# Kernel optimization log

Hardware: AMD Instinct MI355X
Metric: run time of the kernel (lower is better)

The kernel has to match this reference:

```python
import jax, jax.numpy as jnp
import numpy as np

B, S, D, H, L, DFF, WIN = 2, 2048, 768, 12, 2, 3072, 512
EPS = 1e-5
DH = D // H


def setup_inputs() -> dict:
    key = jax.random.key(0)
    ks = jax.random.split(key, 8)
    rn = lambda k, shape: jax.random.normal(k, shape, jnp.float32) * 0.02
    inp = {
        "src": jax.random.normal(ks[0], (B, S, D), jnp.float32),
        "qw": rn(ks[1], (L, D, D)), "qb": jnp.zeros((L, D), jnp.float32),
        "kw": rn(ks[2], (L, D, D)), "kb": jnp.zeros((L, D), jnp.float32),
        "vw": rn(ks[3], (L, D, D)), "vb": jnp.zeros((L, D), jnp.float32),
        "ow": rn(ks[4], (L, D, D)), "ob": jnp.zeros((L, D), jnp.float32),
        "w1": rn(ks[5], (L, DFF, D)), "b1": jnp.zeros((L, DFF), jnp.float32),
        "w2": rn(ks[6], (L, D, DFF)), "b2": jnp.zeros((L, D), jnp.float32),
        "g1": jnp.ones((L, D), jnp.float32), "be1": jnp.zeros((L, D), jnp.float32),
        "g2": jnp.ones((L, D), jnp.float32), "be2": jnp.zeros((L, D), jnp.float32),
    }
    return inp


def _ln(x, g, b):
    m = jnp.mean(x, axis=-1, keepdims=True)
    v = jnp.mean(jnp.square(x - m), axis=-1, keepdims=True)
    return (x - m) * jax.lax.rsqrt(v + EPS) * g + b


def _encoder(src, qw, qb, kw, kb, vw, vb, ow, ob, w1, b1, w2, b2, g1, be1, g2, be2):
    scale = DH ** -0.5
    idx = jnp.arange(S)
    # non-causal sliding window: |i - j| <= window_size // 2
    band = jnp.abs(idx[:, None] - idx[None, :]) <= (WIN // 2)
    neg = -jnp.finfo(jnp.float32).max
    x = src
    for l in range(L):
        # projections -> (B, H, S, DH)
        q = (x @ qw[l].T + qb[l]).reshape(B, S, H, DH).transpose(0, 2, 1, 3)
        k = (x @ kw[l].T + kb[l]).reshape(B, S, H, DH).transpose(0, 2, 1, 3)
        v = (x @ vw[l].T + vb[l]).reshape(B, S, H, DH).transpose(0, 2, 1, 3)
        # full dense scores then band mask (faithful to the original module)
        sim = jnp.einsum('bhid,bhjd->bhij', q * scale, k)
        sim = jnp.where(band, sim, neg)
        attn = jax.nn.softmax(sim, axis=-1)
        o = jnp.einsum('bhij,bhjd->bhid', attn, v)
        o = o.transpose(0, 2, 1, 3).reshape(B, S, D) @ ow[l].T + ob[l]
        # post-norm transformer block (norm_first=False)
        x = _ln(x + o, g1[l], be1[l])
        ff = jax.nn.relu(x @ w1[l].T + b1[l]) @ w2[l].T + b2[l]
        x = _ln(x + ff, g2[l], be2[l])
    return x


def reference(src, qw, qb, kw, kb, vw, vb, ow, ob, w1, b1, w2, b2, g1, be1, g2, be2):
    return _encoder(src, qw, qb, kw, kb, vw, vb, ow, ob, w1, b1, w2, b2, g1, be1, g2, be2)
```

## Files before the change

### kernel.cpp

```cpp
#include <hip/hip_runtime.h>
#include <math.h>

#define BATCH 2
#define SEQ   2048
#define DM    768
#define NHD   12
#define NL    2
#define DFF   3072
#define DH    64
#define HW    256
#define MR    (BATCH*SEQ)
#define EPSF  1e-5f
#define SCALE 0.125f
#define QKVS  2304

typedef __attribute__((ext_vector_type(8))) __bf16 bf16x8;
typedef __attribute__((ext_vector_type(4))) float  f32x4;

__device__ __forceinline__ ushort f2bu(float f) {
    union { __bf16 h; ushort u; } c;
    c.h = (__bf16)f;
    return c.u;
}
__device__ __forceinline__ float bu2f(ushort u) {
    union { uint u; float f; } c;
    c.u = ((uint)u) << 16;
    return c.f;
}

__device__ __forceinline__ void gload16(const ushort* g, ushort* l) {
    __builtin_amdgcn_global_load_lds(
        (const __attribute__((address_space(1))) void*)g,
        (__attribute__((address_space(3))) void*)l, 16, 0, 0);
}

__device__ __forceinline__ void xcd_swz(int& bx, int& by, int& bz) {
    const int gx = gridDim.x, gy = gridDim.y;
    const int nwg = gx * gy * gridDim.z;
    int lin = bx + gx * (by + gy * bz);
    lin = (lin & 7) * (nwg >> 3) + (lin >> 3);
    bx = lin % gx;
    int rest = lin / gx;
    by = rest % gy;
    bz = rest / gy;
}

__global__ __launch_bounds__(256) void cvt(const float* __restrict__ in,
                                           ushort* __restrict__ out, int n)
{
    int i = (blockIdx.x * 256 + threadIdx.x) * 4;
    if (i >= n) return;
    float4 v = *(const float4*)(in + i);
    ushort4 o;
    o.x = f2bu(v.x); o.y = f2bu(v.y); o.z = f2bu(v.z); o.w = f2bu(v.w);
    *(ushort4*)(out + i) = o;
}

__global__ __launch_bounds__(256) void gemm128(
    const ushort* __restrict__ A, const ushort* __restrict__ W,
    const float* __restrict__ bias, ushort* __restrict__ C,
    int M, int N, int K, int relu)
{
    __shared__ ushort As[128 * 32];
    __shared__ ushort Ws[128 * 32];

    int bxi = blockIdx.x, byi = blockIdx.y, bzi = blockIdx.z;
    xcd_swz(bxi, byi, bzi);

    const int t  = threadIdx.x;
    const int bm = byi * 128;
    const int bn = bxi * 128;

    const int w    = t >> 6;
    const int lane = t & 63;
    const int quad = lane >> 4;
    const int lrow = lane & 15;
    const int wm   = (w >> 1) * 64;
    const int wn   = (w & 1) * 64;

    const int srow = t >> 2;
    const int scol = (t & 3) * 8;
    const ushort* ag = A + (size_t)(bm + srow) * K + scol;
    const ushort* wg = W + (size_t)(bn + srow) * K + scol;
    ushort* la0 = &As[t * 8];
    ushort* la1 = &As[2048 + t * 8];
    ushort* lw0 = &Ws[t * 8];
    ushort* lw1 = &Ws[2048 + t * 8];

    f32x4 acc[4][4] = {};

    for (int k0 = 0; k0 < K; k0 += 32) {
        gload16(ag + k0,                  la0);
        gload16(ag + (size_t)64 * K + k0, la1);
        gload16(wg + k0,                  lw0);
        gload16(wg + (size_t)64 * K + k0, lw1);
        __syncthreads();

        bf16x8 af[4], bfr[4];
#pragma unroll
        for (int i = 0; i < 4; ++i)
            af[i] = *(const bf16x8*)&As[(wm + i * 16 + lrow) * 32 + quad * 8];
#pragma unroll
        for (int j = 0; j < 4; ++j)
            bfr[j] = *(const bf16x8*)&Ws[(wn + j * 16 + lrow) * 32 + quad * 8];

#pragma unroll
        for (int i = 0; i < 4; ++i)
#pragma unroll
            for (int j = 0; j < 4; ++j)
                acc[i][j] = __builtin_amdgcn_mfma_f32_16x16x32_bf16(
                    af[i], bfr[j], acc[i][j], 0, 0, 0);
        __syncthreads();
    }

#pragma unroll
    for (int j = 0; j < 4; ++j) {
        const int col = bn + wn + j * 16 + lrow;
        const float bv = bias[col];
#pragma unroll
        for (int i = 0; i < 4; ++i) {
            const int rb = bm + wm + i * 16 + quad * 4;
#pragma unroll
            for (int r = 0; r < 4; ++r) {
                float vv = acc[i][j][r] + bv;
                if (relu) vv = fmaxf(vv, 0.f);
                C[(size_t)(rb + r) * N + col] = f2bu(vv);
            }
        }
    }
}

__global__ __launch_bounds__(256) void gemm64(
    const ushort* __restrict__ A, const ushort* __restrict__ W,
    const float* __restrict__ bias, ushort* __restrict__ C,
    float* __restrict__ part, int M, int N, int Kc, int ldk, int relu)
{
    __shared__ ushort As[64 * 32];
    __shared__ ushort Ws[128 * 32];

    int bxi = blockIdx.x, byi = blockIdx.y, bzi = blockIdx.z;
    xcd_swz(bxi, byi, bzi);

    const int t  = threadIdx.x;
    const int bm = byi * 64;
    const int bn = bxi * 128;
    const int z  = bzi;
    const int kbase = z * Kc;

    const int w    = t >> 6;
    const int lane = t & 63;
    const int quad = lane >> 4;
    const int lrow = lane & 15;
    const int wm   = (w >> 1) * 32;
    const int wn   = (w & 1) * 64;

    const int srow = t >> 2;
    const int scol = (t & 3) * 8;
    const ushort* ag = A + (size_t)(bm + srow) * ldk + kbase + scol;
    const ushort* wg = W + (size_t)(bn + srow) * ldk + kbase + scol;
    ushort* la0 = &As[t * 8];
    ushort* lw0 = &Ws[t * 8];
    ushort* lw1 = &Ws[2048 + t * 8];

    f32x4 acc[2][4] = {};

    for (int k0 = 0; k0 < Kc; k0 += 32) {
        gload16(ag + k0,                    la0);
        gload16(wg + k0,                    lw0);
        gload16(wg + (size_t)64 * ldk + k0, lw1);
        __syncthreads();

        bf16x8 af[2], bfr[4];
#pragma unroll
        for (int i = 0; i < 2; ++i)
            af[i] = *(const bf16x8*)&As[(wm + i * 16 + lrow) * 32 + quad * 8];
#pragma unroll
        for (int j = 0; j < 4; ++j)
            bfr[j] = *(const bf16x8*)&Ws[(wn + j * 16 + lrow) * 32 + quad * 8];

#pragma unroll
        for (int i = 0; i < 2; ++i)
#pragma unroll
            for (int j = 0; j < 4; ++j)
                acc[i][j] = __builtin_amdgcn_mfma_f32_16x16x32_bf16(
                    af[i], bfr[j], acc[i][j], 0, 0, 0);
        __syncthreads();
    }

    if (gridDim.z > 1) {
        float* po = part + (size_t)z * M * N;
#pragma unroll
        for (int j = 0; j < 4; ++j) {
            const int col = bn + wn + j * 16 + lrow;
#pragma unroll
            for (int i = 0; i < 2; ++i) {
                const int rb = bm + wm + i * 16 + quad * 4;
#pragma unroll
                for (int r = 0; r < 4; ++r)
                    po[(size_t)(rb + r) * N + col] = acc[i][j][r];
            }
        }
    } else {
#pragma unroll
        for (int j = 0; j < 4; ++j) {
            const int col = bn + wn + j * 16 + lrow;
            const float bv = bias[col];
#pragma unroll
            for (int i = 0; i < 2; ++i) {
                const int rb = bm + wm + i * 16 + quad * 4;
#pragma unroll
                for (int r = 0; r < 4; ++r) {
                    float vv = acc[i][j][r] + bv;
                    if (relu) vv = fmaxf(vv, 0.f);
                    C[(size_t)(rb + r) * N + col] = f2bu(vv);
                }
            }
        }
    }
}

__global__ __launch_bounds__(256) void red_sk(
    const float* __restrict__ p, const float* __restrict__ bias,
    ushort* __restrict__ out)
{
    const int i = (blockIdx.x * 256 + threadIdx.x) * 4;
    float4 a = *(const float4*)(p + i);
    float4 b = *(const float4*)(p + (size_t)MR * DM + i);
    const int col = i % DM;
    float4 bv = *(const float4*)(bias + col);
    ushort4 o;
    o.x = f2bu(a.x + b.x + bv.x);
    o.y = f2bu(a.y + b.y + bv.y);
    o.z = f2bu(a.z + b.z + bv.z);
    o.w = f2bu(a.w + b.w + bv.w);
    *(ushort4*)(out + i) = o;
}

#define QT  64
#define NCH 9
#define KP  72

__global__ __launch_bounds__(256) void attn(
    const ushort* __restrict__ q, const ushort* __restrict__ k,
    const ushort* __restrict__ v, ushort* __restrict__ o)
{
    __shared__ ushort kv[2][64][KP];
    __shared__ ushort vt[2][64][KP];
    __shared__ ushort sc[QT][KP];

    int bxi = blockIdx.x, byi = blockIdx.y, bzi = blockIdx.z;
    xcd_swz(bxi, byi, bzi);

    const int t    = threadIdx.x;
    const int i0   = bxi * QT;
    const int h    = byi;
    const int b    = bzi;
    const size_t ibase = (size_t)b * SEQ * QKVS + (size_t)h * DH;
    const size_t obase = (size_t)b * SEQ * DM   + (size_t)h * DH;

    const int w    = t >> 6;
    const int lane = t & 63;
    const int quad = lane >> 4;
    const int lrow = lane & 15;
    const int qrow = w * 16;

    const int jstart = i0 - HW;

    const int sjj[2] = { t >> 3, (t + 256) >> 3 };
    const int sd0[2] = { (t & 7) * 8, (t & 7) * 8 };

#pragma unroll
    for (int e = 0; e < 2; ++e) {
        int idx = t + 256 * e;
        int qi = idx >> 3, d0 = (idx & 7) * 8;
        uint4 raw = *(const uint4*)(q + ibase + (size_t)(i0 + qi) * QKVS + d0);
        *(uint4*)&sc[qi][d0] = raw;
    }
    uint4 kr[2], vr[2];
#pragma unroll
    for (int e = 0; e < 2; ++e) {
        int j = jstart + sjj[e];
        kr[e] = make_uint4(0, 0, 0, 0);
        vr[e] = make_uint4(0, 0, 0, 0);
        if (j >= 0 && j < SEQ) {
            kr[e] = *(const uint4*)(k + ibase + (size_t)j * QKVS + sd0[e]);
            vr[e] = *(const uint4*)(v + ibase + (size_t)j * QKVS + sd0[e]);
        }
    }
#pragma unroll
    for (int e = 0; e < 2; ++e) {
        *(uint4*)&kv[0][sjj[e]][sd0[e]] = kr[e];
        const ushort* u = (const ushort*)&vr[e];
#pragma unroll
        for (int x = 0; x < 8; ++x) {
            int dh  = sd0[e] + x;
            int blk = ((sjj[e] >> 3) ^ (dh >> 3)) & 7;
            vt[0][dh][blk * 8 + (sjj[e] & 7)] = u[x];
        }
    }
    __syncthreads();

    const bf16x8 a0 = *(const bf16x8*)&sc[qrow + lrow][quad * 8];
    const bf16x8 a1 = *(const bf16x8*)&sc[qrow + lrow][32 + quad * 8];

    float m_r[4], l_r[4];
    f32x4 oacc[4] = {};
#pragma unroll
    for (int r = 0; r < 4; ++r) { m_r[r] = -1e20f; l_r[r] = 0.f; }

    for (int c = 0; c < NCH; ++c) {
        const int cur = c & 1;
        const int j0  = jstart + c * 64;

        if (c + 1 < NCH) {
            const int j0n = jstart + (c + 1) * 64;
#pragma unroll
            for (int e = 0; e < 2; ++e) {
                int j = j0n + sjj[e];
                kr[e] = make_uint4(0, 0, 0, 0);
                vr[e] = make_uint4(0, 0, 0, 0);
                if (j >= 0 && j < SEQ) {
                    kr[e] = *(const uint4*)(k + ibase + (size_t)j * QKVS + sd0[e]);
                    vr[e] = *(const uint4*)(v + ibase + (size_t)j * QKVS + sd0[e]);
                }
            }
        }

        float p[4][4];
#pragma unroll
        for (int kt = 0; kt < 4; ++kt) {
            const int krow = kt * 16;
            bf16x8 b0 = *(const bf16x8*)&kv[cur][krow + lrow][quad * 8];
            bf16x8 b1 = *(const bf16x8*)&kv[cur][krow + lrow][32 + quad * 8];
            f32x4 acc = {};
            acc = __builtin_amdgcn_mfma_f32_16x16x32_bf16(a0, b0, acc, 0, 0, 0);
            acc = __builtin_amdgcn_mfma_f32_16x16x32_bf16(a1, b1, acc, 0, 0, 0);
            const int jg = j0 + krow + lrow;
#pragma unroll
            for (int r = 0; r < 4; ++r) {
                const int ig = i0 + qrow + quad * 4 + r;
                bool ok = (jg >= 0) && (jg < SEQ) &&
                          (jg >= ig - HW) && (jg <= ig + HW);
                p[kt][r] = ok ? acc[r] * SCALE : -1e30f;
            }
        }

#pragma unroll
        for (int r = 0; r < 4; ++r) {
            float cm = fmaxf(fmaxf(p[0][r], p[1][r]), fmaxf(p[2][r], p[3][r]));
#pragma unroll
            for (int off = 8; off; off >>= 1) cm = fmaxf(cm, __shfl_xor(cm, off));
            const float mn = fmaxf(m_r[r], cm);
            const float f  = __expf(m_r[r] - mn);
            m_r[r] = mn;
            float cs = 0.f;
#pragma unroll
            for (int kt = 0; kt < 4; ++kt) {
                float e = __expf(p[kt][r] - mn);
                p[kt][r] = e;
                cs += e;
            }
#pragma unroll
            for (int off = 8; off; off >>= 1) cs += __shfl_xor(cs, off);
            l_r[r] = l_r[r] * f + cs;
#pragma unroll
            for (int nt = 0; nt < 4; ++nt) oacc[nt][r] *= f;
        }

#pragma unroll
        for (int kt = 0; kt < 4; ++kt)
#pragma unroll
            for (int r = 0; r < 4; ++r)
                sc[qrow + quad * 4 + r][kt * 16 + lrow] = f2bu(p[kt][r]);

        bf16x8 pa0 = *(const bf16x8*)&sc[qrow + lrow][quad * 8];
        bf16x8 pa1 = *(const bf16x8*)&sc[qrow + lrow][32 + quad * 8];
#pragma unroll
        for (int nt = 0; nt < 4; ++nt) {
            const int dh  = nt * 16 + lrow;
            const int rsw = (dh >> 3) & 7;
            bf16x8 b0 = *(const bf16x8*)&vt[cur][dh][((quad)     ^ rsw) * 8];
            bf16x8 b1 = *(const bf16x8*)&vt[cur][dh][((quad + 4) ^ rsw) * 8];
            oacc[nt] = __builtin_amdgcn_mfma_f32_16x16x32_bf16(pa0, b0, oacc[nt], 0, 0, 0);
            oacc[nt] = __builtin_amdgcn_mfma_f32_16x16x32_bf16(pa1, b1, oacc[nt], 0, 0, 0);
        }

        if (c + 1 < NCH) {
            const int nxt = cur ^ 1;
#pragma unroll
            for (int e = 0; e < 2; ++e) {
                *(uint4*)&kv[nxt][sjj[e]][sd0[e]] = kr[e];
                const ushort* u = (const ushort*)&vr[e];
#pragma unroll
                for (int x = 0; x < 8; ++x) {
                    int dh  = sd0[e] + x;
                    int blk = ((sjj[e] >> 3) ^ (dh >> 3)) & 7;
                    vt[nxt][dh][blk * 8 + (sjj[e] & 7)] = u[x];
                }
            }
        }
        __syncthreads();
    }

#pragma unroll
    for (int r = 0; r < 4; ++r) {
        const float inv = 1.f / l_r[r];
        const int qi = i0 + qrow + quad * 4 + r;
#pragma unroll
        for (int nt = 0; nt < 4; ++nt)
            o[obase + (size_t)qi * DM + nt * 16 + lrow] = f2bu(oacc[nt][r] * inv);
    }
}

__global__ __launch_bounds__(256) void add_ln(
    const ushort* __restrict__ xa, const ushort* __restrict__ yb,
    const float* __restrict__ g, const float* __restrict__ be,
    ushort* __restrict__ ob, float* __restrict__ of, int fin)
{
    const int r = blockIdx.x * 4 + (threadIdx.x >> 6);
    const int t = threadIdx.x & 63;
    const size_t off = (size_t)r * DM;
    float sv[12];
    float s1 = 0.f, s2 = 0.f;
#pragma unroll
    for (int ii = 0; ii < 12; ++ii) {
        float vv = bu2f(xa[off + t + 64 * ii]) + bu2f(yb[off + t + 64 * ii]);
        sv[ii] = vv; s1 += vv; s2 += vv * vv;
    }
#pragma unroll
    for (int o2 = 32; o2; o2 >>= 1) {
        s1 += __shfl_xor(s1, o2);
        s2 += __shfl_xor(s2, o2);
    }
    const float mean = s1 * (1.f / 768.f);
    const float rstd = rsqrtf(s2 * (1.f / 768.f) - mean * mean + EPSF);
#pragma unroll
    for (int ii = 0; ii < 12; ++ii) {
        const int c = t + 64 * ii;
        float v = (sv[ii] - mean) * rstd * g[c] + be[c];
        if (fin) of[off + c] = v;
        else     ob[off + c] = f2bu(v);
    }
}

extern "C" void kernel_launch(void* const* d_in, const int* in_sizes, int n_in,
                              void* d_out, int out_size, void* d_ws, size_t ws_size,
                              hipStream_t stream) {
    (void)in_sizes; (void)n_in; (void)out_size; (void)ws_size;
    const float* src = (const float*)d_in[0];
    const float* qw  = (const float*)d_in[1];
    const float* qb  = (const float*)d_in[2];
    const float* kw  = (const float*)d_in[3];
    const float* kb  = (const float*)d_in[4];
    const float* vw  = (const float*)d_in[5];
    const float* vb  = (const float*)d_in[6];
    const float* ow  = (const float*)d_in[7];
    const float* ob  = (const float*)d_in[8];
    const float* w1  = (const float*)d_in[9];
    const float* b1  = (const float*)d_in[10];
    const float* w2  = (const float*)d_in[11];
    const float* b2  = (const float*)d_in[12];
    const float* g1  = (const float*)d_in[13];
    const float* be1 = (const float*)d_in[14];
    const float* g2  = (const float*)d_in[15];
    const float* be2 = (const float*)d_in[16];

    const size_t A    = (size_t)MR * DM;
    const size_t WD1  = (size_t)DM * DM;
    const size_t WQKV = (size_t)3 * DM * DM;
    const size_t WF1  = (size_t)DFF * DM;
    const size_t WF   = (size_t)NL * WF1;

    float*  bcat = (float*)d_ws;
    ushort* p    = (ushort*)(bcat + (size_t)NL * QKVS);
    ushort* qkvwB = p; p += (size_t)NL * WQKV;
    ushort* owB   = p; p += (size_t)NL * WD1;
    ushort* w1B   = p; p += WF;
    ushort* w2B   = p; p += WF;
    ushort* xb    = p; p += A;
    ushort* qkvB  = p; p += 3 * A;
    ushort* oB    = p; p += A;
    ushort* yB    = p; p += A;
    ushort* h1    = p; p += A;
    ushort* ffh   = p;

    float* part = (float*)qkvB;

    for (int l = 0; l < NL; ++l) {
        hipMemcpyAsync(bcat + (size_t)l * QKVS + 0,    qb + (size_t)l * DM,
                       DM * sizeof(float), hipMemcpyDeviceToDevice, stream);
        hipMemcpyAsync(bcat + (size_t)l * QKVS + DM,   kb + (size_t)l * DM,
                       DM * sizeof(float), hipMemcpyDeviceToDevice, stream);
        hipMemcpyAsync(bcat + (size_t)l * QKVS + 2*DM, vb + (size_t)l * DM,
                       DM * sizeof(float), hipMemcpyDeviceToDevice, stream);
    }

    for (int l = 0; l < NL; ++l) {
        cvt<<<(int)(WD1 / 1024), 256, 0, stream>>>(
            qw + (size_t)l * WD1, qkvwB + (size_t)l * WQKV + 0,     (int)WD1);
        cvt<<<(int)(WD1 / 1024), 256, 0, stream>>>(
            kw + (size_t)l * WD1, qkvwB + (size_t)l * WQKV + WD1,   (int)WD1);
        cvt<<<(int)(WD1 / 1024), 256, 0, stream>>>(
            vw + (size_t)l * WD1, qkvwB + (size_t)l * WQKV + 2*WD1, (int)WD1);
    }
    cvt<<<(int)(NL * WD1 / 1024), 256, 0, stream>>>(ow, owB, (int)(NL * WD1));
    cvt<<<(int)(WF / 1024), 256, 0, stream>>>(w1, w1B, (int)WF);
    cvt<<<(int)(WF / 1024), 256, 0, stream>>>(w2, w2B, (int)WF);
    cvt<<<(int)(A  / 1024), 256, 0, stream>>>(src, xb, (int)A);

    const dim3 gQKV(QKVS / 128, MR / 128);
    const dim3 gO(DM / 128, MR / 64);
    const dim3 gF1(DFF / 128, MR / 128);
    const dim3 gF2(DM / 128, MR / 64, 2);
    const dim3 gA(SEQ / QT, NHD, BATCH);

    for (int l = 0; l < NL; ++l) {
        const size_t bD = (size_t)l * DM;
        const size_t bF = (size_t)l * DFF;

        gemm128<<<gQKV, 256, 0, stream>>>(xb, qkvwB + (size_t)l * WQKV,
                                          bcat + (size_t)l * QKVS, qkvB,
                                          MR, QKVS, DM, 0);
        attn<<<gA, 256, 0, stream>>>(qkvB, qkvB + DM, qkvB + 2 * DM, oB);
        gemm64<<<gO, 256, 0, stream>>>(oB, owB + (size_t)l * WD1, ob + bD, yB,
                                       nullptr, MR, DM, DM, DM, 0);
        add_ln<<<MR / 4, 256, 0, stream>>>(xb, yB, g1 + bD, be1 + bD,
                                           h1, nullptr, 0);
        gemm128<<<gF1, 256, 0, stream>>>(h1, w1B + (size_t)l * WF1, b1 + bF, ffh,
                                         MR, DFF, DM, 1);
        gemm64<<<gF2, 256, 0, stream>>>(ffh, w2B + (size_t)l * WF1, nullptr,
                                        nullptr, part, MR, DM, DFF / 2, DFF, 0);
        red_sk<<<(int)(A / 1024), 256, 0, stream>>>(part, b2 + bD, xb);
        if (l == NL - 1)
            add_ln<<<MR / 4, 256, 0, stream>>>(h1, xb, g2 + bD, be2 + bD,
                                               nullptr, (float*)d_out, 1);
        else
            add_ln<<<MR / 4, 256, 0, stream>>>(h1, xb, g2 + bD, be2 + bD,
                                               xb, nullptr, 0);
    }
}
```

Baseline: 498.3 us.

## Double-buffer GEMM shared tiles and fuse split-K reduction into layernorm

Both GEMM kernels now use two shared-memory buffers, so the next K-slice is loaded while MFMAs run on the current one, and one barrier per iteration is removed. The separate split-K reduction kernel is dropped: the second add+layernorm now reads both fp32 partials plus the bias directly. This removes one launch and a bf16 round trip per layer. It doubles LDS use per block, which may reduce occupancy, and it skips the bf16 rounding of the FFN output before the residual add.

Result: faster. 477.5 us (-4.2%).

```diff
diff --git a/kernel.cpp b/kernel.cpp
--- a/kernel.cpp
+++ b/kernel.cpp
@@ -61,8 +61,8 @@
     const float* __restrict__ bias, ushort* __restrict__ C,
     int M, int N, int K, int relu)
 {
-    __shared__ ushort As[128 * 32];
-    __shared__ ushort Ws[128 * 32];
+    __shared__ ushort As[2][128 * 32];
+    __shared__ ushort Ws[2][128 * 32];
 
     int bxi = blockIdx.x, byi = blockIdx.y, bzi = blockIdx.z;
     xcd_swz(bxi, byi, bzi);
@@ -82,27 +82,32 @@
     const int scol = (t & 3) * 8;
     const ushort* ag = A + (size_t)(bm + srow) * K + scol;
     const ushort* wg = W + (size_t)(bn + srow) * K + scol;
-    ushort* la0 = &As[t * 8];
-    ushort* la1 = &As[2048 + t * 8];
-    ushort* lw0 = &Ws[t * 8];
-    ushort* lw1 = &Ws[2048 + t * 8];
 
     f32x4 acc[4][4] = {};
 
+    gload16(ag,                  &As[0][t * 8]);
+    gload16(ag + (size_t)64 * K, &As[0][2048 + t * 8]);
+    gload16(wg,                  &Ws[0][t * 8]);
+    gload16(wg + (size_t)64 * K, &Ws[0][2048 + t * 8]);
+    __syncthreads();
+
+    int cur = 0;
     for (int k0 = 0; k0 < K; k0 += 32) {
-        gload16(ag + k0,                  la0);
-        gload16(ag + (size_t)64 * K + k0, la1);
-        gload16(wg + k0,                  lw0);
-        gload16(wg + (size_t)64 * K + k0, lw1);
-        __syncthreads();
+        const int nxt = cur ^ 1;
+        if (k0 + 32 < K) {
+            gload16(ag + k0 + 32,                  &As[nxt][t * 8]);
+            gload16(ag + (size_t)64 * K + k0 + 32, &As[nxt][2048 + t * 8]);
+            gload16(wg + k0 + 32,                  &Ws[nxt][t * 8]);
+            gload16(wg + (size_t)64 * K + k0 + 32, &Ws[nxt][2048 + t * 8]);
+        }
 
         bf16x8 af[4], bfr[4];
 #pragma unroll
         for (int i = 0; i < 4; ++i)
-            af[i] = *(const bf16x8*)&As[(wm + i * 16 + lrow) * 32 + quad * 8];
+            af[i] = *(const bf16x8*)&As[cur][(wm + i * 16 + lrow) * 32 + quad * 8];
 #pragma unroll
         for (int j = 0; j < 4; ++j)
-            bfr[j] = *(const bf16x8*)&Ws[(wn + j * 16 + lrow) * 32 + quad * 8];
+            bfr[j] = *(const bf16x8*)&Ws[cur][(wn + j * 16 + lrow) * 32 + quad * 8];
 
 #pragma unroll
         for (int i = 0; i < 4; ++i)
@@ -111,6 +116,7 @@
                 acc[i][j] = __builtin_amdgcn_mfma_f32_16x16x32_bf16(
                     af[i], bfr[j], acc[i][j], 0, 0, 0);
         __syncthreads();
+        cur = nxt;
     }
 
 #pragma unroll
@@ -135,8 +141,8 @@
     const float* __restrict__ bias, ushort* __restrict__ C,
     float* __restrict__ part, int M, int N, int Kc, int ldk, int relu)
 {
-    __shared__ ushort As[64 * 32];
-    __shared__ ushort Ws[128 * 32];
+    __shared__ ushort As[2][64 * 32];
+    __shared__ ushort Ws[2][128 * 32];
 
     int bxi = blockIdx.x, byi = blockIdx.y, bzi = blockIdx.z;
     xcd_swz(bxi, byi, bzi);
@@ -158,25 +164,30 @@
     const int scol = (t & 3) * 8;
     const ushort* ag = A + (size_t)(bm + srow) * ldk + kbase + scol;
     const ushort* wg = W + (size_t)(bn + srow) * ldk + kbase + scol;
-    ushort* la0 = &As[t * 8];
-    ushort* lw0 = &Ws[t * 8];
-    ushort* lw1 = &Ws[2048 + t * 8];
 
     f32x4 acc[2][4] = {};
 
+    gload16(ag,                    &As[0][t * 8]);
+    gload16(wg,                    &Ws[0][t * 8]);
+    gload16(wg + (size_t)64 * ldk, &Ws[0][2048 + t * 8]);
+    __syncthreads();
+
+    int cur = 0;
     for (int k0 = 0; k0 < Kc; k0 += 32) {
-        gload16(ag + k0,                    la0);
-        gload16(wg + k0,                    lw0);
-        gload16(wg + (size_t)64 * ldk + k0, lw1);
-        __syncthreads();
+        const int nxt = cur ^ 1;
+        if (k0 + 32 < Kc) {
+            gload16(ag + k0 + 32,                    &As[nxt][t * 8]);
+            gload16(wg + k0 + 32,                    &Ws[nxt][t * 8]);
+            gload16(wg + (size_t)64 * ldk + k0 + 32, &Ws[nxt][2048 + t * 8]);
+        }
 
         bf16x8 af[2], bfr[4];
 #pragma unroll
         for (int i = 0; i < 2; ++i)
-            af[i] = *(const bf16x8*)&As[(wm + i * 16 + lrow) * 32 + quad * 8];
+            af[i] = *(const bf16x8*)&As[cur][(wm + i * 16 + lrow) * 32 + quad * 8];
 #pragma unroll
         for (int j = 0; j < 4; ++j)
-            bfr[j] = *(const bf16x8*)&Ws[(wn + j * 16 + lrow) * 32 + quad * 8];
+            bfr[j] = *(const bf16x8*)&Ws[cur][(wn + j * 16 + lrow) * 32 + quad * 8];
 
 #pragma unroll
         for (int i = 0; i < 2; ++i)
@@ -185,6 +196,7 @@
                 acc[i][j] = __builtin_amdgcn_mfma_f32_16x16x32_bf16(
                     af[i], bfr[j], acc[i][j], 0, 0, 0);
         __syncthreads();
+        cur = nxt;
     }
 
     if (gridDim.z > 1) {
@@ -217,23 +229,6 @@
             }
         }
     }
-}
-
-__global__ __launch_bounds__(256) void red_sk(
-    const float* __restrict__ p, const float* __restrict__ bias,
-    ushort* __restrict__ out)
-{
-    const int i = (blockIdx.x * 256 + threadIdx.x) * 4;
-    float4 a = *(const float4*)(p + i);
-    float4 b = *(const float4*)(p + (size_t)MR * DM + i);
-    const int col = i % DM;
-    float4 bv = *(const float4*)(bias + col);
-    ushort4 o;
-    o.x = f2bu(a.x + b.x + bv.x);
-    o.y = f2bu(a.y + b.y + bv.y);
-    o.z = f2bu(a.z + b.z + bv.z);
-    o.w = f2bu(a.w + b.w + bv.w);
-    *(ushort4*)(out + i) = o;
 }
 
 #define QT  64
@@ -425,6 +420,40 @@
 #pragma unroll
     for (int ii = 0; ii < 12; ++ii) {
         float vv = bu2f(xa[off + t + 64 * ii]) + bu2f(yb[off + t + 64 * ii]);
+        sv[ii] = vv; s1 += vv; s2 += vv * vv;
+    }
+#pragma unroll
+    for (int o2 = 32; o2; o2 >>= 1) {
+        s1 += __shfl_xor(s1, o2);
+        s2 += __shfl_xor(s2, o2);
+    }
+    const float mean = s1 * (1.f / 768.f);
+    const float rstd = rsqrtf(s2 * (1.f / 768.f) - mean * mean + EPSF);
+#pragma unroll
+    for (int ii = 0; ii < 12; ++ii) {
+        const int c = t + 64 * ii;
+        float v = (sv[ii] - mean) * rstd * g[c] + be[c];
+        if (fin) of[off + c] = v;
+        else     ob[off + c] = f2bu(v);
+    }
+}
+
+__global__ __launch_bounds__(256) void add_ln_sk(
+    const ushort* __restrict__ xa, const float* __restrict__ pp,
+    const float* __restrict__ bias, const float* __restrict__ g,
+    const float* __restrict__ be,
+    ushort* __restrict__ ob, float* __restrict__ of, int fin)
+{
+    const int r = blockIdx.x * 4 + (threadIdx.x >> 6);
+    const int t = threadIdx.x & 63;
+    const size_t off = (size_t)r * DM;
+    float sv[12];
+    float s1 = 0.f, s2 = 0.f;
+#pragma unroll
+    for (int ii = 0; ii < 12; ++ii) {
+        const int c = t + 64 * ii;
+        float vv = bu2f(xa[off + c]) + pp[off + c]
+                 + pp[(size_t)MR * DM + off + c] + bias[c];
         sv[ii] = vv; s1 += vv; s2 += vv * vv;
     }
 #pragma unroll
@@ -530,12 +559,13 @@
                                          MR, DFF, DM, 1);
         gemm64<<<gF2, 256, 0, stream>>>(ffh, w2B + (size_t)l * WF1, nullptr,
                                         nullptr, part, MR, DM, DFF / 2, DFF, 0);
-        red_sk<<<(int)(A / 1024), 256, 0, stream>>>(part, b2 + bD, xb);
         if (l == NL - 1)
-            add_ln<<<MR / 4, 256, 0, stream>>>(h1, xb, g2 + bD, be2 + bD,
-                                               nullptr, (float*)d_out, 1);
+            add_ln_sk<<<MR / 4, 256, 0, stream>>>(h1, part, b2 + bD,
+                                                  g2 + bD, be2 + bD,
+                                                  nullptr, (float*)d_out, 1);
         else
-            add_ln<<<MR / 4, 256, 0, stream>>>(h1, xb, g2 + bD, be2 + bD,
-                                               xb, nullptr, 0);
-    }
-}
+            add_ln_sk<<<MR / 4, 256, 0, stream>>>(h1, part, b2 + bD,
+                                                  g2 + bD, be2 + bD,
+                                                  xb, nullptr, 0);
+    }
+}
```
